# Kernel tuning notes

Measured on AMD Instinct MI355X. Metric: run time of the kernel, lower is better.

## Reference

```python
import jax, jax.numpy as jnp
from jax import lax
import numpy as np

VOCAB, L, D, K = 50000, 8921, 300, 10
B, T = 8, 2048


def setup_inputs() -> dict:
    key = jax.random.key(0)
    k_ids, k_e, k_cw, k_cb, k_u = jax.random.split(key, 5)
    ids = jax.random.randint(k_ids, (B, T), 0, VOCAB, dtype=jnp.int32)
    embed_w = jax.random.normal(k_e, (VOCAB, D), dtype=jnp.float32) * 0.02
    embed_w = embed_w.at[0].set(0.0)  # padding_idx=0
    conv_w = jax.random.normal(k_cw, (D, D, K), dtype=jnp.float32) * 0.02  # (out, in, k) == torch OIH
    conv_b = jax.random.normal(k_cb, (D,), dtype=jnp.float32) * 0.02
    U = jax.random.normal(k_u, (L, D), dtype=jnp.float32)
    fc_bias = jnp.zeros((L,), dtype=jnp.float32)
    return {"ids": ids, "embed_w": embed_w, "conv_w": conv_w, "conv_b": conv_b, "U": U, "fc_bias": fc_bias}


def reference(ids, embed_w, conv_w, conv_b, U, fc_bias):
    # Embedding lookup (padding_idx row already zeroed in table)
    e = embed_w[ids]                       # (B, T, D)
    x = jnp.transpose(e, (0, 2, 1))        # (B, D, T)
    pad = conv_w.shape[-1] - 1             # torch padding=filter_size-1 (both sides)
    h = lax.conv_general_dilated(
        x, conv_w, window_strides=(1,), padding=[(pad, pad)],
        dimension_numbers=("NCH", "OIH", "NCH"))
    h = jax.nn.relu(h + conv_b[None, :, None])   # (B, D, T') where T' = T + K - 1
    attn = jax.nn.softmax(jnp.einsum("ld,bdt->blt", U, h), axis=-1)  # (B, L, T')
    z = jnp.einsum("blt,bdt->bld", attn, h)                          # (B, L, D)
    logits = jnp.einsum("bld,ld->bl", z, U) + fc_bias                # (B, L)
    return logits
```

## Files before the change

### kernel.cpp

```cpp
#include <hip/hip_runtime.h>

#define VOCAB   50000
#define LDIM    8921
#define DDIM    300
#define DPAD    320
#define KSZ     10
#define BATCH   8
#define TSEQ    2048
#define PADL    9
#define TPRIME  2057
#define TPADDED 2066
#define LPAD    8928

#define TSTG    32
#define NTT     65
#define TALLOC  (NTT * TSTG)
#define LBLK    70

typedef short s8v __attribute__((ext_vector_type(8)));
typedef float f4v __attribute__((ext_vector_type(4)));

typedef const __attribute__((address_space(1))) unsigned int* gas_ptr;
typedef __attribute__((address_space(3))) unsigned int* las_ptr;

__device__ inline unsigned short f2bf(float f) {
  union { float f; unsigned u; } v; v.f = f;
  unsigned r = v.u + 0x7FFF + ((v.u >> 16) & 1);
  return (unsigned short)(r >> 16);
}

__global__ __launch_bounds__(256) void prep_kernel(
    const float* __restrict__ w, const float* __restrict__ U,
    unsigned short* __restrict__ wT, unsigned short* __restrict__ Ub) {
  int bid = blockIdx.x;
  if (bid < KSZ * DPAD) {
    int k = bid / DPAD, o = bid % DPAD;
    for (int i = threadIdx.x; i < DPAD; i += 256) {
      float v = (o < DDIM && i < DDIM) ? w[((size_t)o * DDIM + i) * KSZ + k] : 0.0f;
      wT[((size_t)k * DPAD + o) * DPAD + i] = f2bf(v);
    }
  } else {
    int l = bid - KSZ * DPAD;
    for (int d = threadIdx.x; d < DPAD; d += 256) {
      float v = (l < LDIM && d < DDIM) ? U[(size_t)l * DDIM + d] : 0.0f;
      Ub[(size_t)l * DPAD + d] = f2bf(v);
    }
  }
}

#define CTN 80
#define CROWS 89
#define CSTRIDE 328
__global__ __launch_bounds__(256) void conv_mfma_kernel(
    const int* __restrict__ ids, const float* __restrict__ embed_w,
    const unsigned short* __restrict__ wT,
    const float* __restrict__ bias, unsigned short* __restrict__ h) {
  __shared__ unsigned short xls[CROWS * CSTRIDE];
  int b = blockIdx.x & 7, tb = blockIdx.x >> 3;
  int t0 = tb * CTN;
  int tid = threadIdx.x;
  {
    const int* idsb = ids + b * TSEQ;
    for (int idx = tid; idx < CROWS * 40; idx += 256) {
      int rr = idx / 40, c8 = idx % 40;
      int tau = t0 + rr;
      bool inr = (tau >= PADL) && (tau < PADL + TSEQ);
      unsigned short pk[8];
      if (inr) {
        int row = idsb[tau - PADL];
        const float* src = embed_w + (size_t)row * DDIM + c8 * 8;
        float4 lo = (c8 * 8 + 3 < DDIM) ? *(const float4*)&src[0] : make_float4(0, 0, 0, 0);
        float4 hi = (c8 * 8 + 7 < DDIM) ? *(const float4*)&src[4] : make_float4(0, 0, 0, 0);
        pk[0] = f2bf(lo.x); pk[1] = f2bf(lo.y); pk[2] = f2bf(lo.z); pk[3] = f2bf(lo.w);
        pk[4] = f2bf(hi.x); pk[5] = f2bf(hi.y); pk[6] = f2bf(hi.z); pk[7] = f2bf(hi.w);
      } else {
#pragma unroll
        for (int e = 0; e < 8; ++e) pk[e] = 0;
      }
      *(int4*)&xls[rr * CSTRIDE + c8 * 8] = *(const int4*)pk;
    }
  }
  __syncthreads();
  int w = tid >> 6, lane = tid & 63;
  int l15 = lane & 15, quad = lane >> 4;
  int ob = w * 80;
  f4v acc[5][5];
#pragma unroll
  for (int mf = 0; mf < 5; ++mf) {
    float bv[4];
#pragma unroll
    for (int rr = 0; rr < 4; ++rr) {
      int o = ob + mf * 16 + quad * 4 + rr;
      bv[rr] = (o < DDIM) ? bias[o] : 0.0f;
    }
#pragma unroll
    for (int nf = 0; nf < 5; ++nf) {
      acc[mf][nf][0] = bv[0]; acc[mf][nf][1] = bv[1];
      acc[mf][nf][2] = bv[2]; acc[mf][nf][3] = bv[3];
    }
  }
  const unsigned short* wl = wT + (size_t)(ob + l15) * DPAD + quad * 8;
  s8v Aping[5], Apong[5];
#pragma unroll
  for (int mf = 0; mf < 5; ++mf) Aping[mf] = *(const s8v*)&wl[mf * 16 * DPAD];
#pragma unroll
  for (int mf = 0; mf < 5; ++mf) Apong[mf] = *(const s8v*)&wl[mf * 16 * DPAD + 32];
  for (int ii = 0; ii < 100; ii += 2) {
    {
      int kc = ii / 10, it = ii % 10;
      s8v Bv[5];
#pragma unroll
      for (int nf = 0; nf < 5; ++nf)
        Bv[nf] = *(const s8v*)&xls[(nf * 16 + l15 + kc) * CSTRIDE + it * 32 + quad * 8];
#pragma unroll
      for (int mf = 0; mf < 5; ++mf)
#pragma unroll
        for (int nf = 0; nf < 5; ++nf)
          acc[mf][nf] = __builtin_amdgcn_mfma_f32_16x16x32_bf16(Aping[mf], Bv[nf], acc[mf][nf], 0, 0, 0);
      int p = ii + 2;
      if (p < 100) {
        int kp = p / 10, itp = p % 10;
        const unsigned short* wp = wl + (size_t)kp * (DPAD * DPAD) + itp * 32;
#pragma unroll
        for (int mf = 0; mf < 5; ++mf) Aping[mf] = *(const s8v*)&wp[mf * 16 * DPAD];
      }
    }
    {
      int kc = (ii + 1) / 10, it = (ii + 1) % 10;
      s8v Bv[5];
#pragma unroll
      for (int nf = 0; nf < 5; ++nf)
        Bv[nf] = *(const s8v*)&xls[(nf * 16 + l15 + kc) * CSTRIDE + it * 32 + quad * 8];
#pragma unroll
      for (int mf = 0; mf < 5; ++mf)
#pragma unroll
        for (int nf = 0; nf < 5; ++nf)
          acc[mf][nf] = __builtin_amdgcn_mfma_f32_16x16x32_bf16(Apong[mf], Bv[nf], acc[mf][nf], 0, 0, 0);
      int p = ii + 3;
      if (p < 100) {
        int kp = p / 10, itp = p % 10;
        const unsigned short* wp = wl + (size_t)kp * (DPAD * DPAD) + itp * 32;
#pragma unroll
        for (int mf = 0; mf < 5; ++mf) Apong[mf] = *(const s8v*)&wp[mf * 16 * DPAD];
      }
    }
  }
#pragma unroll
  for (int mf = 0; mf < 5; ++mf) {
    int obase = ob + mf * 16 + quad * 4;
#pragma unroll
    for (int nf = 0; nf < 5; ++nf) {
      int t = t0 + nf * 16 + l15;
      bool live = t < TPRIME;
      unsigned short pk[4];
#pragma unroll
      for (int rr = 0; rr < 4; ++rr)
        pk[rr] = live ? f2bf(fmaxf(acc[mf][nf][rr], 0.0f)) : (unsigned short)0;
      *(uint2*)&h[((size_t)b * TALLOC + t) * DPAD + obase] = *(uint2*)pk;
    }
  }
}

__global__ __launch_bounds__(256, 3) void attn_mfma_kernel(
    const unsigned short* __restrict__ h, const unsigned short* __restrict__ Ub,
    const float* __restrict__ fcb, float* __restrict__ out) {
  __shared__ unsigned short hls[2 * TSTG * DPAD];
  int b = blockIdx.x & 7, lb = blockIdx.x >> 3;
  int tid = threadIdx.x;
  int w = tid >> 6, lane = tid & 63;
  int l15 = lane & 15, quad = lane >> 4;
  const unsigned short* hb = h + (size_t)b * TALLOC * DPAD;

  s8v A[2][10];
  {
    int lr0 = lb * 128 + w * 32 + l15;
#pragma unroll
    for (int mf = 0; mf < 2; ++mf) {
      int lr = lr0 + mf * 16;
      if (lr >= LPAD) lr = LPAD - 1;
      const unsigned short* up = Ub + (size_t)lr * DPAD + quad * 8;
#pragma unroll
      for (int kc = 0; kc < 10; ++kc)
        A[mf][kc] = *(const s8v*)&up[kc * 32];
    }
  }

  int srcoff[5];
#pragma unroll
  for (int j = 0; j < 5; ++j) {
    int g = w * 320 + j * 64 + lane;
    int r = g / 40, c = g % 40;
    srcoff[j] = r * DPAD + ((c ^ (r & 7)) * 8);
  }

#pragma unroll
  for (int j = 0; j < 5; ++j)
    __builtin_amdgcn_global_load_lds((gas_ptr)(const void*)(hb + srcoff[j]),
                                     (las_ptr)(void*)&hls[w * 2560 + j * 512],
                                     16, 0, 0);
  asm volatile("s_waitcnt vmcnt(0)" ::: "memory");
  __builtin_amdgcn_s_barrier();

  float se[2][4], sw[2][4];
#pragma unroll
  for (int mf = 0; mf < 2; ++mf)
#pragma unroll
    for (int r = 0; r < 4; ++r) { se[mf][r] = 0.0f; sw[mf][r] = 0.0f; }

  int xr8 = (l15 & 7) * 8;
  int rowb0 = l15 * DPAD;
  int rowb1 = (16 + l15) * DPAD;
  int bufsel = 0;
  const f4v vzero = {0.0f, 0.0f, 0.0f, 0.0f};
  for (int t = 0; t < NTT; ++t) {
    if (t + 1 < NTT) {
      const unsigned short* src = hb + (size_t)(t + 1) * TSTG * DPAD;
      int dstb = (bufsel ^ 1) * 10240 + w * 2560;
#pragma unroll
      for (int j = 0; j < 5; ++j)
        __builtin_amdgcn_global_load_lds((gas_ptr)(const void*)(src + srcoff[j]),
                                         (las_ptr)(void*)&hls[dstb + j * 512],
                                         16, 0, 0);
    }
    const unsigned short* bufc = &hls[bufsel * 10240];
    f4v a00, a01, a10, a11;
    __builtin_amdgcn_s_setprio(1);
    {
      int ko = (quad * 8) ^ xr8;
      s8v Bv0 = *(const s8v*)&bufc[rowb0 + ko];
      s8v Bv1 = *(const s8v*)&bufc[rowb1 + ko];
      a00 = __builtin_amdgcn_mfma_f32_16x16x32_bf16(A[0][0], Bv0, vzero, 0, 0, 0);
      a01 = __builtin_amdgcn_mfma_f32_16x16x32_bf16(A[0][0], Bv1, vzero, 0, 0, 0);
      a10 = __builtin_amdgcn_mfma_f32_16x16x32_bf16(A[1][0], Bv0, vzero, 0, 0, 0);
      a11 = __builtin_amdgcn_mfma_f32_16x16x32_bf16(A[1][0], Bv1, vzero, 0, 0, 0);
    }
#pragma unroll
    for (int kc = 1; kc < 10; ++kc) {
      int ko = (kc * 32 + quad * 8) ^ xr8;
      s8v Bv0 = *(const s8v*)&bufc[rowb0 + ko];
      s8v Bv1 = *(const s8v*)&bufc[rowb1 + ko];
      a00 = __builtin_amdgcn_mfma_f32_16x16x32_bf16(A[0][kc], Bv0, a00, 0, 0, 0);
      a01 = __builtin_amdgcn_mfma_f32_16x16x32_bf16(A[0][kc], Bv1, a01, 0, 0, 0);
      a10 = __builtin_amdgcn_mfma_f32_16x16x32_bf16(A[1][kc], Bv0, a10, 0, 0, 0);
      a11 = __builtin_amdgcn_mfma_f32_16x16x32_bf16(A[1][kc], Bv1, a11, 0, 0, 0);
    }
    __builtin_amdgcn_s_setprio(0);
#pragma unroll
    for (int r = 0; r < 4; ++r) {
      float s0 = a00[r], s1 = a01[r];
      float e0 = __expf(s0), e1 = __expf(s1);
      se[0][r] += e0 + e1;
      sw[0][r] = fmaf(e0, s0, sw[0][r]);
      sw[0][r] = fmaf(e1, s1, sw[0][r]);
      float s2 = a10[r], s3 = a11[r];
      float e2 = __expf(s2), e3 = __expf(s3);
      se[1][r] += e2 + e3;
      sw[1][r] = fmaf(e2, s2, sw[1][r]);
      sw[1][r] = fmaf(e3, s3, sw[1][r]);
    }
    asm volatile("s_waitcnt vmcnt(0)" ::: "memory");
    __builtin_amdgcn_s_barrier();
    bufsel ^= 1;
  }

#pragma unroll
  for (int mf = 0; mf < 2; ++mf)
#pragma unroll
    for (int r = 0; r < 4; ++r) {
      float a = se[mf][r], c = sw[mf][r];
#pragma unroll
      for (int off = 1; off < 16; off <<= 1) {
        a += __shfl_xor(a, off, 64);
        c += __shfl_xor(c, off, 64);
      }
      if (l15 == 0) {
        int l = lb * 128 + w * 32 + mf * 16 + quad * 4 + r;
        if (l < LDIM) out[(size_t)b * LDIM + l] = c / (a - 23.0f) + fcb[l];
      }
    }
}

extern "C" void kernel_launch(void* const* d_in, const int* in_sizes, int n_in,
                              void* d_out, int out_size, void* d_ws, size_t ws_size,
                              hipStream_t stream) {
  const int*   ids     = (const int*)d_in[0];
  const float* embed_w = (const float*)d_in[1];
  const float* conv_w  = (const float*)d_in[2];
  const float* conv_b  = (const float*)d_in[3];
  const float* U       = (const float*)d_in[4];
  const float* fc_bias = (const float*)d_in[5];
  float* out = (float*)d_out;

  unsigned char* p = (unsigned char*)d_ws;
  unsigned short* hb = (unsigned short*)p;                 p += (size_t)BATCH * TALLOC * DPAD * 2;
  unsigned short* wT = (unsigned short*)p;                 p += (size_t)KSZ * DPAD * DPAD * 2;
  unsigned short* Ub = (unsigned short*)p;

  hipLaunchKernelGGL(prep_kernel, dim3(KSZ * DPAD + LPAD), dim3(256), 0, stream,
                     conv_w, U, wT, Ub);
  hipLaunchKernelGGL(conv_mfma_kernel, dim3(BATCH * 26), dim3(256), 0, stream,
                     ids, embed_w, wT, conv_b, hb);
  hipLaunchKernelGGL(attn_mfma_kernel, dim3(BATCH * LBLK), dim3(256), 0, stream,
                     hb, Ub, fc_bias, out);
}
```

Baseline: 283.8 us.

## Split conv reduction dimension across two wave groups with LDS reduction

The conv kernel now launches 512 threads per block. Two groups of four waves each handle half of the 100 K-chunks (kernel tap by input-channel slices). Partial accumulators from the second group are written to shared memory, reusing the input tile buffer, and added by the first group before ReLU and the bf16 store. This doubles the waves per block to raise MFMA and latency-hiding parallelism on a grid of only 208 blocks, at the cost of extra syncs, LDS traffic for the reduction, and register pressure under the 512x2 launch bound.

```diff
diff --git a/kernel.cpp b/kernel.cpp
--- a/kernel.cpp
+++ b/kernel.cpp
@@ -51,7 +51,7 @@
 #define CTN 80
 #define CROWS 89
 #define CSTRIDE 328
-__global__ __launch_bounds__(256) void conv_mfma_kernel(
+__global__ __launch_bounds__(512, 2) void conv_mfma_kernel(
     const int* __restrict__ ids, const float* __restrict__ embed_w,
     const unsigned short* __restrict__ wT,
     const float* __restrict__ bias, unsigned short* __restrict__ h) {
@@ -61,7 +61,7 @@
   int tid = threadIdx.x;
   {
     const int* idsb = ids + b * TSEQ;
-    for (int idx = tid; idx < CROWS * 40; idx += 256) {
+    for (int idx = tid; idx < CROWS * 40; idx += 512) {
       int rr = idx / 40, c8 = idx % 40;
       int tau = t0 + rr;
       bool inr = (tau >= PADL) && (tau < PADL + TSEQ);
@@ -81,9 +81,10 @@
     }
   }
   __syncthreads();
-  int w = tid >> 6, lane = tid & 63;
+  int ww = tid >> 6, lane = tid & 63;
+  int wo = ww & 3, wk = ww >> 2;
   int l15 = lane & 15, quad = lane >> 4;
-  int ob = w * 80;
+  int ob = wo * 80;
   f4v acc[5][5];
 #pragma unroll
   for (int mf = 0; mf < 5; ++mf) {
@@ -91,7 +92,7 @@
 #pragma unroll
     for (int rr = 0; rr < 4; ++rr) {
       int o = ob + mf * 16 + quad * 4 + rr;
-      bv[rr] = (o < DDIM) ? bias[o] : 0.0f;
+      bv[rr] = (wk == 0 && o < DDIM) ? bias[o] : 0.0f;
     }
 #pragma unroll
     for (int nf = 0; nf < 5; ++nf) {
@@ -100,12 +101,18 @@
     }
   }
   const unsigned short* wl = wT + (size_t)(ob + l15) * DPAD + quad * 8;
+  int ii0 = wk * 50, iiE = ii0 + 50;
   s8v Aping[5], Apong[5];
-#pragma unroll
-  for (int mf = 0; mf < 5; ++mf) Aping[mf] = *(const s8v*)&wl[mf * 16 * DPAD];
-#pragma unroll
-  for (int mf = 0; mf < 5; ++mf) Apong[mf] = *(const s8v*)&wl[mf * 16 * DPAD + 32];
-  for (int ii = 0; ii < 100; ii += 2) {
+  {
+    int kc0 = ii0 / 10;
+#pragma unroll
+    for (int mf = 0; mf < 5; ++mf)
+      Aping[mf] = *(const s8v*)&wl[(size_t)kc0 * (DPAD * DPAD) + mf * 16 * DPAD];
+#pragma unroll
+    for (int mf = 0; mf < 5; ++mf)
+      Apong[mf] = *(const s8v*)&wl[(size_t)kc0 * (DPAD * DPAD) + mf * 16 * DPAD + 32];
+  }
+  for (int ii = ii0; ii < iiE; ii += 2) {
     {
       int kc = ii / 10, it = ii % 10;
       s8v Bv[5];
@@ -118,7 +125,7 @@
         for (int nf = 0; nf < 5; ++nf)
           acc[mf][nf] = __builtin_amdgcn_mfma_f32_16x16x32_bf16(Aping[mf], Bv[nf], acc[mf][nf], 0, 0, 0);
       int p = ii + 2;
-      if (p < 100) {
+      if (p < iiE) {
         int kp = p / 10, itp = p % 10;
         const unsigned short* wp = wl + (size_t)kp * (DPAD * DPAD) + itp * 32;
 #pragma unroll
@@ -137,7 +144,7 @@
         for (int nf = 0; nf < 5; ++nf)
           acc[mf][nf] = __builtin_amdgcn_mfma_f32_16x16x32_bf16(Apong[mf], Bv[nf], acc[mf][nf], 0, 0, 0);
       int p = ii + 3;
-      if (p < 100) {
+      if (p < iiE) {
         int kp = p / 10, itp = p % 10;
         const unsigned short* wp = wl + (size_t)kp * (DPAD * DPAD) + itp * 32;
 #pragma unroll
@@ -145,18 +152,39 @@
       }
     }
   }
-#pragma unroll
-  for (int mf = 0; mf < 5; ++mf) {
-    int obase = ob + mf * 16 + quad * 4;
-#pragma unroll
-    for (int nf = 0; nf < 5; ++nf) {
-      int t = t0 + nf * 16 + l15;
-      bool live = t < TPRIME;
-      unsigned short pk[4];
-#pragma unroll
-      for (int rr = 0; rr < 4; ++rr)
-        pk[rr] = live ? f2bf(fmaxf(acc[mf][nf][rr], 0.0f)) : (unsigned short)0;
-      *(uint2*)&h[((size_t)b * TALLOC + t) * DPAD + obase] = *(uint2*)pk;
+  float* red = (float*)xls;
+#pragma unroll
+  for (int p = 0; p < 2; ++p) {
+    __syncthreads();
+    if (wk == 1 && (wo >> 1) == p) {
+      float* dst = red + (wo & 1) * 6400;
+#pragma unroll
+      for (int mf = 0; mf < 5; ++mf)
+#pragma unroll
+        for (int nf = 0; nf < 5; ++nf)
+#pragma unroll
+          for (int rr = 0; rr < 4; ++rr)
+            dst[(mf * 16 + quad * 4 + rr) * 80 + nf * 16 + l15] = acc[mf][nf][rr];
+    }
+    __syncthreads();
+    if (wk == 0 && (wo >> 1) == p) {
+      const float* srcp = red + (wo & 1) * 6400;
+#pragma unroll
+      for (int mf = 0; mf < 5; ++mf) {
+        int obase = ob + mf * 16 + quad * 4;
+#pragma unroll
+        for (int nf = 0; nf < 5; ++nf) {
+          int t = t0 + nf * 16 + l15;
+          bool live = t < TPRIME;
+          unsigned short pk[4];
+#pragma unroll
+          for (int rr = 0; rr < 4; ++rr) {
+            float v = acc[mf][nf][rr] + srcp[(mf * 16 + quad * 4 + rr) * 80 + nf * 16 + l15];
+            pk[rr] = live ? f2bf(fmaxf(v, 0.0f)) : (unsigned short)0;
+          }
+          *(uint2*)&h[((size_t)b * TALLOC + t) * DPAD + obase] = *(uint2*)pk;
+        }
+      }
     }
   }
 }
@@ -298,7 +326,7 @@
 
   hipLaunchKernelGGL(prep_kernel, dim3(KSZ * DPAD + LPAD), dim3(256), 0, stream,
                      conv_w, U, wT, Ub);
-  hipLaunchKernelGGL(conv_mfma_kernel, dim3(BATCH * 26), dim3(256), 0, stream,
+  hipLaunchKernelGGL(conv_mfma_kernel, dim3(BATCH * 26), dim3(512), 0, stream,
                      ids, embed_w, wT, conv_b, hb);
   hipLaunchKernelGGL(attn_mfma_kernel, dim3(BATCH * LBLK), dim3(256), 0, stream,
                      hb, Ub, fc_bias, out);
```

After: 290.7 us. 1.02x slower.
